# Optimization experiments

Measured on AMD Instinct MI355X. Metric: run time of the kernel, lower is better.

## Reference

```python
import jax, jax.numpy as jnp
import numpy as np

EPS = 1e-6
BETA = 0.5
B, T, N = 128, 30, 10000   # batch, BP iterations, n error bits
M, K = 5000, 10            # checks, observables
CHK_W, OBS_W = 6, 50       # row weights of chkmat / obsmat


def _make_supports():
    """Deterministic sparse supports (CSR-style flattened col indices + row ids)."""
    rng = np.random.default_rng(0)
    chk_rows = np.argpartition(rng.random((M, N)), CHK_W, axis=1)[:, :CHK_W]
    obs_rows = np.argpartition(rng.random((K, N)), OBS_W, axis=1)[:, :OBS_W]
    chk_idx = chk_rows.reshape(-1).astype(np.int32)
    chk_seg = np.repeat(np.arange(M, dtype=np.int32), CHK_W)
    obs_idx = obs_rows.reshape(-1).astype(np.int32)
    obs_seg = np.repeat(np.arange(K, dtype=np.int32), OBS_W)
    return chk_idx, chk_seg, obs_idx, obs_seg


def setup_inputs() -> dict:
    key = jax.random.key(0)
    k1, k2, k3 = jax.random.split(key, 3)
    all_llrs = jax.random.normal(k1, (B, T, N), dtype=jnp.float32) * 2.0
    syndromes = jax.random.randint(k2, (B, M), 0, 2, dtype=jnp.int32)
    observables = jax.random.randint(k3, (B, K), 0, 2, dtype=jnp.int32)
    chk_idx, chk_seg, obs_idx, obs_seg = _make_supports()
    return {
        "all_llrs": all_llrs,
        "syndromes": syndromes,
        "observables": observables,
        "chk_idx": jnp.asarray(chk_idx),
        "chk_seg": jnp.asarray(chk_seg),
        "obs_idx": jnp.asarray(obs_idx),
        "obs_seg": jnp.asarray(obs_seg),
    }


def _pred_llr(t, idx, seg, num_seg):
    # t: (B,T,N) tanh(llr/2); gather support cols -> (B,T,E)
    g = t[:, :, idx]
    # segmented product over support entries (tanh rule), segments on axis 0
    p = jax.ops.segment_prod(jnp.moveaxis(g, 2, 0), seg, num_segments=num_seg)  # (S,B,T)
    p = jnp.clip(jnp.moveaxis(p, 0, 2), -1.0 + EPS, 1.0 - EPS)  # (B,T,S)
    return 2.0 * jnp.arctanh(p)


def _bce_with_logits(z, y):
    # stable BCEWithLogits: max(z,0) - z*y + log(1+exp(-|z|)) == logaddexp(0,z) - z*y
    return jnp.logaddexp(0.0, z) - z * y


def reference(all_llrs, syndromes, observables, chk_idx, chk_seg, obs_idx, obs_seg):
    t = jnp.tanh(all_llrs * 0.5)                                   # (B,T,N)
    syn_llr = _pred_llr(t, chk_idx, chk_seg, syndromes.shape[1])    # (B,T,M)
    obs_llr = _pred_llr(t, obs_idx, obs_seg, observables.shape[1])  # (B,T,K)
    y_syn = syndromes.astype(jnp.float32)[:, None, :]
    y_obs = observables.astype(jnp.float32)[:, None, :]
    loss1 = _bce_with_logits(-syn_llr, y_syn).sum(axis=2)           # (B,T)
    loss2 = _bce_with_logits(-obs_llr, y_obs).sum(axis=2)           # (B,T)
    loss = BETA * loss1 + (1.0 - BETA) * loss2
    return loss.mean()
```

## Files before the change

kernel.cpp:

```cpp
#include <hip/hip_runtime.h>
#include <hip/hip_fp16.h>

#define B_  128
#define T_  30
#define N_  10000
#define M_  5000
#define K_  10
#define CHK_W_ 6
#define OBS_W_ 50
#define EPS_ 1e-6f
#define LOG2F_ 0.69314718056f
#define BT_ (B_*T_)
#define RG_ 128
#define NGRP_ (BT_/RG_)
#define CHUNK_ 100
#define NCHK_BLK_ (M_/CHUNK_)

__global__ __launch_bounds__(256) void tanh_transpose_kernel(
    const float* __restrict__ llrs,
    __half*      __restrict__ tt)
{
    __shared__ float tile[64][65];
    const int bt0 = blockIdx.x * 64;
    const int n0  = blockIdx.y * 64;
    const int tid = threadIdx.x;
    const int c   = tid & 63;
    const int r4  = tid >> 6;

    if (n0 + c < N_) {
        #pragma unroll
        for (int i = 0; i < 16; ++i) {
            int r = i * 4 + r4;
            float v = llrs[(size_t)(bt0 + r) * N_ + (n0 + c)];
            tile[r][c] = 1.f - 2.f / (__expf(v) + 1.f);
        }
    }
    __syncthreads();

    const int r = tid & 63;
    #pragma unroll
    for (int i = 0; i < 16; ++i) {
        int cc = i * 4 + r4;
        if (n0 + cc < N_)
            tt[(size_t)(n0 + cc) * BT_ + (bt0 + r)] = __float2half(tile[r][cc]);
    }
}

__global__ __launch_bounds__(256) void gather_loss_kernel(
    const __half* __restrict__ tt,
    const int*    __restrict__ syndromes,
    const int*    __restrict__ observables,
    const int*    __restrict__ chk_idx,
    const int*    __restrict__ obs_idx,
    float*        __restrict__ out)
{
    const int tid  = threadIdx.x;
    const int lane = tid & 63;
    const int wave = tid >> 6;
    const int bt0  = blockIdx.x * RG_;
    const int r0   = bt0 + 2 * lane;
    const int b0   = r0 / T_;
    const int b1   = (r0 + 1) / T_;
    const __half2* tt2 = (const __half2*)tt;
    const int half_off = r0 >> 1;

    float acc = 0.f;
    const int y = blockIdx.y;

    if (y < NCHK_BLK_) {
        const int* syn0 = syndromes + (size_t)b0 * M_;
        const int* syn1 = syndromes + (size_t)b1 * M_;
        const int m0 = y * CHUNK_ + wave * (CHUNK_ / 4);
        #pragma unroll 2
        for (int m = m0; m < m0 + CHUNK_ / 4; ++m) {
            const int* ci = chk_idx + m * CHK_W_;
            __half2 a0 = tt2[(size_t)ci[0] * (BT_/2) + half_off];
            __half2 a1 = tt2[(size_t)ci[1] * (BT_/2) + half_off];
            __half2 a2 = tt2[(size_t)ci[2] * (BT_/2) + half_off];
            __half2 a3 = tt2[(size_t)ci[3] * (BT_/2) + half_off];
            __half2 a4 = tt2[(size_t)ci[4] * (BT_/2) + half_off];
            __half2 a5 = tt2[(size_t)ci[5] * (BT_/2) + half_off];
            __half2 q  = __hmul2(__hmul2(__hmul2(a0, a1), __hmul2(a2, a3)),
                                 __hmul2(a4, a5));
            float p0 = __low2float(q);
            float p1 = __high2float(q);
            p0 = fminf(fmaxf(p0, -1.f + EPS_), 1.f - EPS_);
            p1 = fminf(fmaxf(p1, -1.f + EPS_), 1.f - EPS_);
            float sp0 = syn0[m] ? -p0 : p0;
            float sp1 = syn1[m] ? -p1 : p1;
            acc += (LOG2F_ - __logf(1.f + sp0))
                 + (LOG2F_ - __logf(1.f + sp1));
        }
    } else {
        const int* ob0 = observables + (size_t)b0 * K_;
        const int* ob1 = observables + (size_t)b1 * K_;
        for (int k = wave; k < K_; k += 4) {
            const int* oi = obs_idx + k * OBS_W_;
            __half2 q = __float2half2_rn(1.f);
            #pragma unroll 10
            for (int j = 0; j < OBS_W_; ++j)
                q = __hmul2(q, tt2[(size_t)oi[j] * (BT_/2) + half_off]);
            float p0 = __low2float(q);
            float p1 = __high2float(q);
            p0 = fminf(fmaxf(p0, -1.f + EPS_), 1.f - EPS_);
            p1 = fminf(fmaxf(p1, -1.f + EPS_), 1.f - EPS_);
            float sp0 = ob0[k] ? -p0 : p0;
            float sp1 = ob1[k] ? -p1 : p1;
            acc += (LOG2F_ - __logf(1.f + sp0))
                 + (LOG2F_ - __logf(1.f + sp1));
        }
    }

    __shared__ float red[4];
    #pragma unroll
    for (int off = 32; off > 0; off >>= 1)
        acc += __shfl_down(acc, off, 64);
    if (lane == 0) red[wave] = acc;
    __syncthreads();
    if (tid == 0) {
        float s = red[0] + red[1] + red[2] + red[3];
        atomicAdd(out, s * (0.5f / BT_));
    }
}

extern "C" void kernel_launch(void* const* d_in, const int* in_sizes, int n_in,
                              void* d_out, int out_size, void* d_ws, size_t ws_size,
                              hipStream_t stream) {
    const float* all_llrs    = (const float*)d_in[0];
    const int*   syndromes   = (const int*)d_in[1];
    const int*   observables = (const int*)d_in[2];
    const int*   chk_idx     = (const int*)d_in[3];
    const int*   obs_idx     = (const int*)d_in[5];
    float*  out = (float*)d_out;
    __half* tt  = (__half*)d_ws;

    hipMemsetAsync(out, 0, sizeof(float) * out_size, stream);

    dim3 g1(BT_ / 64, (N_ + 63) / 64);
    tanh_transpose_kernel<<<g1, 256, 0, stream>>>(all_llrs, tt);

    dim3 g2(NGRP_, NCHK_BLK_ + 1);
    gather_loss_kernel<<<g2, 256, 0, stream>>>(
        tt, syndromes, observables, chk_idx, obs_idx, out);
}
```

Before: 288.7 us.

## Store transposed tanh values as packed FP8 in a batch-padded layout

The intermediate tanh table moves from fp16 to FP8, packed with the hardware cvt_pk_fp8 instructions. It is re-laid out so each batch's 30 iterations sit in a 32-slot stride, which lets every lane load 8 consecutive values with one 64-bit gather. The two padding slots are masked out of the loss, and the check chunk size is reduced so more blocks cover the work. This halves the bytes written and gathered through the intermediate buffer. The cost is much coarser precision in the tanh values and in products of up to 50 factors, which may shift the loss beyond tolerance.

```diff
diff --git a/kernel.cpp b/kernel.cpp
--- a/kernel.cpp
+++ b/kernel.cpp
@@ -1,24 +1,23 @@
 #include <hip/hip_runtime.h>
-#include <hip/hip_fp16.h>
+
+typedef float floatx2 __attribute__((ext_vector_type(2)));
 
 #define B_  128
 #define T_  30
 #define N_  10000
 #define M_  5000
 #define K_  10
-#define CHK_W_ 6
 #define OBS_W_ 50
 #define EPS_ 1e-6f
 #define LOG2F_ 0.69314718056f
-#define BT_ (B_*T_)
-#define RG_ 128
-#define NGRP_ (BT_/RG_)
-#define CHUNK_ 100
-#define NCHK_BLK_ (M_/CHUNK_)
+#define BT_  3840
+#define BTP_ 4096
+#define CHUNK_ 40
+#define NCHK_ (M_/CHUNK_)
 
-__global__ __launch_bounds__(256) void tanh_transpose_kernel(
-    const float* __restrict__ llrs,
-    __half*      __restrict__ tt)
+__global__ __launch_bounds__(256) void tanh_transpose_fp8(
+    const float*   __restrict__ llrs,
+    unsigned char* __restrict__ tt)
 {
     __shared__ float tile[64][65];
     const int bt0 = blockIdx.x * 64;
@@ -37,77 +36,106 @@
     }
     __syncthreads();
 
-    const int r = tid & 63;
+    const int pair = tid & 31;
+    const int colg = tid >> 5;
+    const int r    = bt0 + 2 * pair;
+    const int bb   = r / 30;
+    const int pr   = bb * 32 + (r - bb * 30);
     #pragma unroll
-    for (int i = 0; i < 16; ++i) {
-        int cc = i * 4 + r4;
-        if (n0 + cc < N_)
-            tt[(size_t)(n0 + cc) * BT_ + (bt0 + r)] = __float2half(tile[r][cc]);
+    for (int i = 0; i < 8; ++i) {
+        int col = colg + 8 * i;
+        if (n0 + col < N_) {
+            float v0 = tile[2 * pair][col];
+            float v1 = tile[2 * pair + 1][col];
+            int pk = __builtin_amdgcn_cvt_pk_fp8_f32(v0, v1, 0, false);
+            *(unsigned short*)(tt + (size_t)(n0 + col) * BTP_ + pr) =
+                (unsigned short)pk;
+        }
     }
 }
 
-__global__ __launch_bounds__(256) void gather_loss_kernel(
-    const __half* __restrict__ tt,
-    const int*    __restrict__ syndromes,
-    const int*    __restrict__ observables,
-    const int*    __restrict__ chk_idx,
-    const int*    __restrict__ obs_idx,
-    float*        __restrict__ out)
+__device__ __forceinline__ void fold8(uint2 q, float* p, bool first) {
+    floatx2 a0 = __builtin_amdgcn_cvt_pk_f32_fp8((int)q.x, false);
+    floatx2 a1 = __builtin_amdgcn_cvt_pk_f32_fp8((int)q.x, true);
+    floatx2 a2 = __builtin_amdgcn_cvt_pk_f32_fp8((int)q.y, false);
+    floatx2 a3 = __builtin_amdgcn_cvt_pk_f32_fp8((int)q.y, true);
+    if (first) {
+        p[0] = a0.x; p[1] = a0.y; p[2] = a1.x; p[3] = a1.y;
+        p[4] = a2.x; p[5] = a2.y; p[6] = a3.x; p[7] = a3.y;
+    } else {
+        p[0] *= a0.x; p[1] *= a0.y; p[2] *= a1.x; p[3] *= a1.y;
+        p[4] *= a2.x; p[5] *= a2.y; p[6] *= a3.x; p[7] *= a3.y;
+    }
+}
+
+__global__ __launch_bounds__(256) void gather_loss_fp8(
+    const unsigned char* __restrict__ tt,
+    const int*           __restrict__ syndromes,
+    const int*           __restrict__ observables,
+    const int*           __restrict__ chk_idx,
+    const int*           __restrict__ obs_idx,
+    float*               __restrict__ out)
 {
     const int tid  = threadIdx.x;
     const int lane = tid & 63;
     const int wave = tid >> 6;
-    const int bt0  = blockIdx.x * RG_;
-    const int r0   = bt0 + 2 * lane;
-    const int b0   = r0 / T_;
-    const int b1   = (r0 + 1) / T_;
-    const __half2* tt2 = (const __half2*)tt;
-    const int half_off = r0 >> 1;
+    const int r0   = blockIdx.x * 512 + lane * 8;
+    const int b    = r0 >> 5;
+    const int roff = r0 >> 3;
+    const float pmask = ((r0 & 31) == 24) ? 0.f : 1.f;
+    const uint2* tt2 = (const uint2*)tt;
 
     float acc = 0.f;
     const int y = blockIdx.y;
 
-    if (y < NCHK_BLK_) {
-        const int* syn0 = syndromes + (size_t)b0 * M_;
-        const int* syn1 = syndromes + (size_t)b1 * M_;
+    if (y < NCHK_) {
+        const int* syn = syndromes + (size_t)b * M_;
         const int m0 = y * CHUNK_ + wave * (CHUNK_ / 4);
         #pragma unroll 2
         for (int m = m0; m < m0 + CHUNK_ / 4; ++m) {
-            const int* ci = chk_idx + m * CHK_W_;
-            __half2 a0 = tt2[(size_t)ci[0] * (BT_/2) + half_off];
-            __half2 a1 = tt2[(size_t)ci[1] * (BT_/2) + half_off];
-            __half2 a2 = tt2[(size_t)ci[2] * (BT_/2) + half_off];
-            __half2 a3 = tt2[(size_t)ci[3] * (BT_/2) + half_off];
-            __half2 a4 = tt2[(size_t)ci[4] * (BT_/2) + half_off];
-            __half2 a5 = tt2[(size_t)ci[5] * (BT_/2) + half_off];
-            __half2 q  = __hmul2(__hmul2(__hmul2(a0, a1), __hmul2(a2, a3)),
-                                 __hmul2(a4, a5));
-            float p0 = __low2float(q);
-            float p1 = __high2float(q);
-            p0 = fminf(fmaxf(p0, -1.f + EPS_), 1.f - EPS_);
-            p1 = fminf(fmaxf(p1, -1.f + EPS_), 1.f - EPS_);
-            float sp0 = syn0[m] ? -p0 : p0;
-            float sp1 = syn1[m] ? -p1 : p1;
-            acc += (LOG2F_ - __logf(1.f + sp0))
-                 + (LOG2F_ - __logf(1.f + sp1));
+            const int* ci = chk_idx + m * 6;
+            uint2 q0 = tt2[(size_t)ci[0] * (BTP_ / 8) + roff];
+            uint2 q1 = tt2[(size_t)ci[1] * (BTP_ / 8) + roff];
+            uint2 q2 = tt2[(size_t)ci[2] * (BTP_ / 8) + roff];
+            uint2 q3 = tt2[(size_t)ci[3] * (BTP_ / 8) + roff];
+            uint2 q4 = tt2[(size_t)ci[4] * (BTP_ / 8) + roff];
+            uint2 q5 = tt2[(size_t)ci[5] * (BTP_ / 8) + roff];
+            float p[8];
+            fold8(q0, p, true);  fold8(q1, p, false); fold8(q2, p, false);
+            fold8(q3, p, false); fold8(q4, p, false); fold8(q5, p, false);
+            const float sgn = syn[m] ? -1.f : 1.f;
+            float local = 0.f;
+            #pragma unroll
+            for (int j = 0; j < 8; ++j) {
+                float sp = sgn * p[j];
+                sp = fminf(fmaxf(sp, -1.f + EPS_), 1.f - EPS_);
+                float tm = LOG2F_ - __logf(1.f + sp);
+                local += (j < 6) ? tm : tm * pmask;
+            }
+            acc += local;
         }
     } else {
-        const int* ob0 = observables + (size_t)b0 * K_;
-        const int* ob1 = observables + (size_t)b1 * K_;
+        const int* ob = observables + (size_t)b * K_;
         for (int k = wave; k < K_; k += 4) {
             const int* oi = obs_idx + k * OBS_W_;
-            __half2 q = __float2half2_rn(1.f);
-            #pragma unroll 10
-            for (int j = 0; j < OBS_W_; ++j)
-                q = __hmul2(q, tt2[(size_t)oi[j] * (BT_/2) + half_off]);
-            float p0 = __low2float(q);
-            float p1 = __high2float(q);
-            p0 = fminf(fmaxf(p0, -1.f + EPS_), 1.f - EPS_);
-            p1 = fminf(fmaxf(p1, -1.f + EPS_), 1.f - EPS_);
-            float sp0 = ob0[k] ? -p0 : p0;
-            float sp1 = ob1[k] ? -p1 : p1;
-            acc += (LOG2F_ - __logf(1.f + sp0))
-                 + (LOG2F_ - __logf(1.f + sp1));
+            float p[8];
+            uint2 q = tt2[(size_t)oi[0] * (BTP_ / 8) + roff];
+            fold8(q, p, true);
+            #pragma unroll 7
+            for (int j2 = 1; j2 < OBS_W_; ++j2) {
+                uint2 qq = tt2[(size_t)oi[j2] * (BTP_ / 8) + roff];
+                fold8(qq, p, false);
+            }
+            const float sgn = ob[k] ? -1.f : 1.f;
+            float local = 0.f;
+            #pragma unroll
+            for (int j = 0; j < 8; ++j) {
+                float sp = sgn * p[j];
+                sp = fminf(fmaxf(sp, -1.f + EPS_), 1.f - EPS_);
+                float tm = LOG2F_ - __logf(1.f + sp);
+                local += (j < 6) ? tm : tm * pmask;
+            }
+            acc += local;
         }
     }
 
@@ -119,7 +147,7 @@
     __syncthreads();
     if (tid == 0) {
         float s = red[0] + red[1] + red[2] + red[3];
-        atomicAdd(out, s * (0.5f / BT_));
+        atomicAdd(out, s * (0.5f / (float)BT_));
     }
 }
 
@@ -131,15 +159,15 @@
     const int*   observables = (const int*)d_in[2];
     const int*   chk_idx     = (const int*)d_in[3];
     const int*   obs_idx     = (const int*)d_in[5];
-    float*  out = (float*)d_out;
-    __half* tt  = (__half*)d_ws;
+    float*         out = (float*)d_out;
+    unsigned char* tt  = (unsigned char*)d_ws;
 
     hipMemsetAsync(out, 0, sizeof(float) * out_size, stream);
 
     dim3 g1(BT_ / 64, (N_ + 63) / 64);
-    tanh_transpose_kernel<<<g1, 256, 0, stream>>>(all_llrs, tt);
+    tanh_transpose_fp8<<<g1, 256, 0, stream>>>(all_llrs, tt);
 
-    dim3 g2(NGRP_, NCHK_BLK_ + 1);
-    gather_loss_kernel<<<g2, 256, 0, stream>>>(
+    dim3 g2(BTP_ / 512, NCHK_ + 1);
+    gather_loss_fp8<<<g2, 256, 0, stream>>>(
         tt, syndromes, observables, chk_idx, obs_idx, out);
 }
```

After: 285.7 us. About the same (-1.0%).
